# Kernel optimization log

Measured on AMD Instinct MI355X. Metric: run time of the kernel, lower is better.

## Reference

```python
import jax, jax.numpy as jnp
import numpy as np

EPS = 1e-12  # torch F.normalize default eps


def _l2norm(x):
    # F.normalize(x, dim=-1): x / max(||x||_2, eps)
    n = jnp.sqrt(jnp.sum(x * x, axis=-1, keepdims=True))
    return x / jnp.maximum(n, EPS)


def setup_inputs() -> dict:
    key = jax.random.key(0)
    ks = jax.random.split(key, 5)
    n, d, t, h = 16, 1024, 1024, 4
    dh = d // h
    return {
        "rgb": jax.random.normal(ks[0], (n, d, t), dtype=jnp.float32),
        "flow": jax.random.normal(ks[1], (n, d, t), dtype=jnp.float32),
        "rgb_proj": jax.random.normal(ks[2], (h, d, dh), dtype=jnp.float32),
        "flow_proj": jax.random.normal(ks[3], (h, d, dh), dtype=jnp.float32),
        "atte_w": jax.random.normal(ks[4], (h, dh, dh), dtype=jnp.float32),
    }


def reference(rgb, flow, rgb_proj, flow_proj, atte_w):
    # inputs are (n, d, t); module transposes to (n, t, d)
    rgb_t = jnp.swapaxes(rgb, -1, -2)
    flow_t = jnp.swapaxes(flow, -1, -2)
    n, t, d = rgb_t.shape

    # per-head projection + L2 normalize: (n, h, t, dh)
    o_rgb = _l2norm(jnp.einsum('ntd,hde->nhte', rgb_t, rgb_proj))
    o_flow = _l2norm(jnp.einsum('ntd,hde->nhte', flow_t, flow_proj))

    # bilinear attention core: (n, h, t, t)
    att = jnp.einsum('nhte,nhse->nhts', jnp.einsum('nhtd,hde->nhte', o_rgb, atte_w), o_flow)

    rgb_atte = jax.nn.softmax(att, axis=-1)
    flow_atte = jax.nn.softmax(jnp.swapaxes(att, -1, -2), axis=-1)

    e_rgb = jax.nn.gelu(jnp.einsum('nhts,nhsd->nhtd', rgb_atte, o_rgb), approximate=False)
    e_flow = jax.nn.gelu(jnp.einsum('nhts,nhsd->nhtd', flow_atte, o_flow), approximate=False)

    # replicate torch: e.mT.reshape(n, t, -1) (C-order reinterpretation of (n,h,dh,t))
    f_rgb = jnp.tanh(jnp.swapaxes(e_rgb, -1, -2).reshape(n, t, d) + rgb_t)
    f_flow = jnp.tanh(jnp.swapaxes(e_flow, -1, -2).reshape(n, t, d) + flow_t)

    return jnp.swapaxes(f_rgb, -1, -2), jnp.swapaxes(f_flow, -1, -2)
```

## Files before the change

### kernel.cpp

```cpp
#include <hip/hip_runtime.h>
#include <hip/hip_bf16.h>
#include <cstdint>
#include <cstddef>


typedef __bf16 bf16_t;
typedef bf16_t bf16x4 __attribute__((ext_vector_type(4)));
typedef bf16_t bf16x8 __attribute__((ext_vector_type(8)));
typedef float  f32x4  __attribute__((ext_vector_type(4)));

#define DEV static __device__ __forceinline__

constexpr int Tdim = 1024;
constexpr int Ddim = 1024;
constexpr int DH   = 256;
constexpr int NH   = 4;
constexpr int NB   = 16;

DEV f32x4 mm16(bf16x8 a, bf16x8 b, f32x4 c) {
  return __builtin_amdgcn_mfma_f32_16x16x32_bf16(a, b, c, 0, 0, 0);
}

DEV bf16x8 cmb(bf16x4 lo, bf16x4 hi) {
  return __builtin_shufflevector(lo, hi, 0, 1, 2, 3, 4, 5, 6, 7);
}

DEV void tr_pair(const bf16_t* base, int lane, bf16x4& lo, bf16x4& hi) {
  uint32_t a = (uint32_t)(uintptr_t)base + (uint32_t)(lane * 8);
  asm volatile("ds_read_b64_tr_b16 %0, %2\n\t"
               "ds_read_b64_tr_b16 %1, %2 offset:512"
               : "=v"(lo), "=v"(hi)
               : "v"(a));
}

DEV void lgkm0_fence() {
  asm volatile("s_waitcnt lgkmcnt(0)" ::: "memory");
  __builtin_amdgcn_sched_barrier(0);
}

DEV void gload16(const void* g, void* l) {
  __builtin_amdgcn_global_load_lds(
      (const __attribute__((address_space(1))) uint32_t*)g,
      (__attribute__((address_space(3))) uint32_t*)l, 16, 0, 0);
}

DEV float ftanh(float x) {
  float a = __expf(2.0f * x);
  return 1.0f - 2.0f * __builtin_amdgcn_rcpf(a + 1.0f);
}

__global__ void kconvW(const float* __restrict__ rgbp,
                       const float* __restrict__ flowp,
                       const float* __restrict__ attw,
                       bf16_t* __restrict__ Wl, bf16_t* __restrict__ Wa) {
  int bid = blockIdx.x;
  if (bid < 1024) {
    int oc = bid * 256 + threadIdx.x;
    int c = oc & 15, g = (oc >> 4) & 3, nf = (oc >> 6) & 15;
    int kb = (oc >> 10) & 31, h = (oc >> 15) & 3, mod = oc >> 17;
    const float* src = (mod ? flowp : rgbp) + (size_t)h * Ddim * DH + nf * 16 + c;
    bf16x8 v;
#pragma unroll
    for (int i = 0; i < 8; ++i) {
      int k = kb * 32 + ((i < 4) ? 4 * g + i : 12 + 4 * g + i);
      v[i] = (bf16_t)src[(size_t)k * DH];
    }
    *(bf16x8*)(Wl + (size_t)oc * 8) = v;
  } else {
    int oc = (bid - 1024) * 256 + threadIdx.x;
    int c = oc & 15, g = (oc >> 4) & 3, nf = (oc >> 6) & 15;
    int kb = (oc >> 10) & 7, h = oc >> 13;
    const float* src = attw + (size_t)h * DH * DH + nf * 16 + c;
    bf16x8 v;
#pragma unroll
    for (int i = 0; i < 8; ++i) {
      int k = kb * 32 + 8 * g + i;
      v[i] = (bf16_t)src[(size_t)k * DH];
    }
    *(bf16x8*)(Wa + (size_t)oc * 8) = v;
  }
}

__global__ __launch_bounds__(256, 4)
void kproj(const float* __restrict__ rgb, const float* __restrict__ flow,
           const bf16_t* __restrict__ Wl, const bf16_t* __restrict__ Wa,
           bf16_t* __restrict__ o_rgb, bf16_t* __restrict__ o_flow,
           bf16_t* __restrict__ Aout) {
  const int t0  = blockIdx.x * 64;
  const int h   = blockIdx.y;
  const int nn  = blockIdx.z >> 1;
  const int mod = blockIdx.z & 1;
  const float* X = (mod ? flow : rgb) + (size_t)nn * Ddim * Tdim + t0;
  const bf16_t* Wb = Wl + (size_t)(mod * NH + h) * 32 * 8192;
  bf16_t* O = (mod ? o_flow : o_rgb) + (size_t)(nn * NH + h) * Tdim * DH;

  __shared__ __align__(128) bf16_t Alds[64 * 256];
  __shared__ __align__(128) bf16_t AchD[2 * 2048];
  char* WdB = (char*)Alds;
  float* sqp = (float*)AchD;

  const int tid = threadIdx.x;
  const int lane = tid & 63, wv = tid >> 6;
  const int g = lane >> 4, ln = lane & 15;

  f32x4 acc[4][4] = {};
  const int akk = tid >> 3, atoff = (tid & 7) * 8;

  auto stageW = [&](int b, int kb) {
    const char* ws = (const char*)(Wb + (size_t)kb * 8192);
#pragma unroll
    for (int j = 0; j < 4; ++j)
      gload16(ws + j * 4096 + wv * 1024 + lane * 16,
              WdB + b * 16384 + j * 4096 + wv * 1024);
  };

  auto stageX = [&](int b, int kb) {
    const float* srcx = X + (size_t)(kb * 32 + akk) * Tdim + atoff;
    float4 f0 = *(const float4*)srcx;
    float4 f1 = *(const float4*)(srcx + 4);
    bf16x8 v = {(bf16_t)f0.x, (bf16_t)f0.y, (bf16_t)f0.z, (bf16_t)f0.w,
                (bf16_t)f1.x, (bf16_t)f1.y, (bf16_t)f1.z, (bf16_t)f1.w};
    *(bf16x8*)&AchD[b * 2048 + (atoff >> 4) * 512 + akk * 16 + (atoff & 15)] = v;
  };

  stageW(0, 0);
  __builtin_amdgcn_sched_barrier(0);
  stageX(0, 0);
  __syncthreads();

  int cur = 0;
  for (int kb = 0; kb < 32; ++kb) {
    if (kb + 1 < 32) {
      stageW(cur ^ 1, kb + 1);
      __builtin_amdgcn_sched_barrier(0);
      stageX(cur ^ 1, kb + 1);
    }

    bf16x4 alo[4], ahi[4];
#pragma unroll
    for (int mi = 0; mi < 4; ++mi)
      tr_pair(&AchD[cur * 2048 + mi * 512], lane, alo[mi], ahi[mi]);
    bf16x8 wf[4];
#pragma unroll
    for (int f = 0; f < 4; ++f)
      wf[f] = *(const bf16x8*)(WdB + cur * 16384 + (wv * 4 + f) * 1024 +
                               lane * 16);
    lgkm0_fence();
#pragma unroll
    for (int mi = 0; mi < 4; ++mi) {
      bf16x8 a = cmb(alo[mi], ahi[mi]);
#pragma unroll
      for (int f = 0; f < 4; ++f) acc[mi][f] = mm16(a, wf[f], acc[mi][f]);
    }
    __syncthreads();
    cur ^= 1;
  }

  float inv[4][4];
#pragma unroll
  for (int mi = 0; mi < 4; ++mi)
#pragma unroll
    for (int r = 0; r < 4; ++r) {
      float s = 0.f;
#pragma unroll
      for (int f = 0; f < 4; ++f) { float v = acc[mi][f][r]; s += v * v; }
      s += __shfl_xor(s, 1); s += __shfl_xor(s, 2);
      s += __shfl_xor(s, 4); s += __shfl_xor(s, 8);
      if (ln == 0) sqp[wv * 64 + mi * 16 + 4 * g + r] = s;
    }
  __syncthreads();
#pragma unroll
  for (int mi = 0; mi < 4; ++mi)
#pragma unroll
    for (int r = 0; r < 4; ++r) {
      int rl = mi * 16 + 4 * g + r;
      float s = sqp[rl] + sqp[64 + rl] + sqp[128 + rl] + sqp[192 + rl];
      inv[mi][r] = 1.0f / fmaxf(sqrtf(s), 1e-12f);
    }
  __syncthreads();

#pragma unroll
  for (int mi = 0; mi < 4; ++mi)
#pragma unroll
    for (int f = 0; f < 4; ++f)
#pragma unroll
      for (int r = 0; r < 4; ++r) {
        bf16_t val = (bf16_t)(acc[mi][f][r] * inv[mi][r]);
        int row = mi * 16 + 4 * g + r;
        int col = wv * 64 + f * 16 + ln;
        O[(size_t)(t0 + row) * DH + col] = val;
        if (mod == 0)
          *(bf16_t*)((char*)Alds + ((row * 512 + col * 2) ^ ((row & 7) << 4))) = val;
      }

  if (mod != 0) return;

  __syncthreads();
  bf16_t* Ao = Aout + (size_t)(nn * NH + h) * Tdim * DH;
  f32x4 acc2[4][4] = {};
  for (int kb = 0; kb < 8; ++kb) {
    bf16x8 af[4];
#pragma unroll
    for (int mi = 0; mi < 4; ++mi) {
      int row = mi * 16 + ln;
      af[mi] = *(const bf16x8*)((const char*)Alds +
               ((row * 512 + kb * 64 + g * 16) ^ ((row & 7) << 4)));
    }
    bf16x8 wf[4];
    const bf16_t* wt = Wa + (size_t)(h * 8 + kb) * 8192 + (wv * 4) * 512 + lane * 8;
#pragma unroll
    for (int f = 0; f < 4; ++f) wf[f] = *(const bf16x8*)(wt + f * 512);
#pragma unroll
    for (int mi = 0; mi < 4; ++mi)
#pragma unroll
      for (int f = 0; f < 4; ++f) acc2[mi][f] = mm16(af[mi], wf[f], acc2[mi][f]);
  }
#pragma unroll
  for (int mi = 0; mi < 4; ++mi)
#pragma unroll
    for (int f = 0; f < 4; ++f)
#pragma unroll
      for (int r = 0; r < 4; ++r)
        Ao[(size_t)(t0 + mi * 16 + 4 * g + r) * DH + wv * 64 + f * 16 + ln] =
            (bf16_t)acc2[mi][f][r];
}

__global__ __launch_bounds__(256, 2)
void kflash(const bf16_t* __restrict__ o_rgb, const bf16_t* __restrict__ o_flow,
            const bf16_t* __restrict__ Aw,
            const float* __restrict__ rgb, const float* __restrict__ flow,
            float* __restrict__ out) {
  const int bid = blockIdx.x;
  const int p  = (bid & 7) * 16 + (bid >> 6);
  const int qx = (bid >> 3) & 7;
  const int nn = p >> 3, h = (p >> 1) & 3, pass = p & 1;
  const int t0 = qx * 128;
  const size_t nhoff = (size_t)(nn * NH + h) * Tdim * DH;
  const bf16_t* Qp = (pass ? o_flow : Aw) + nhoff;
  const bf16_t* Kp = (pass ? Aw : o_flow) + nhoff;
  const bf16_t* Vp = (pass ? o_flow : o_rgb) + nhoff;
  const float*  Xr = (pass ? flow : rgb) + (size_t)nn * Ddim * Tdim;
  float* Op = out + (size_t)pass * NB * Ddim * Tdim + (size_t)nn * Ddim * Tdim;

  __shared__ __align__(128) bf16_t Klds[2][32 * 256];
  __shared__ __align__(128) bf16_t Vch [2][32 * 256];

  const int tid = threadIdx.x;
  const int lane = tid & 63, wv = tid >> 6;
  const int g = lane >> 4, ln = lane & 15;

  bf16x8 qf[2][8];
#pragma unroll
  for (int rg = 0; rg < 2; ++rg) {
    const bf16_t* qrow = Qp + (size_t)(t0 + wv * 32 + rg * 16 + ln) * DH;
#pragma unroll
    for (int ks = 0; ks < 8; ++ks)
      qf[rg][ks] = *(const bf16x8*)(qrow + ks * 32 + 8 * g);
  }

  auto stage = [&](int b, int s0) {
    const char* Ks = (const char*)Kp + (size_t)s0 * 512;
    const char* Vs = (const char*)Vp + (size_t)s0 * 512;
    char* Kd = (char*)&Klds[b][0] + wv * 1024;
    char* Vd = (char*)&Vch[b][0] + wv * 1024;
#pragma unroll
    for (int j = 0; j < 4; ++j) {
      int gc = j * 256 + tid;
      int d  = gc * 16;
      gload16(Ks + (d ^ (((d >> 9) & 7) << 4)), Kd + j * 4096);
      int ech = gc >> 6, kk = (gc & 63) >> 1, half = gc & 1;
      gload16(Vs + kk * 512 + (ech * 2 + half) * 16, Vd + j * 4096);
    }
  };

  f32x4 eacc[2][16] = {};
  float l_par[2] = {0.f, 0.f};

  stage(0, 0);
  __syncthreads();

  int cur = 0;
  for (int s0 = 0; s0 < Tdim; s0 += 32) {
    if (s0 + 32 < Tdim) stage(cur ^ 1, s0 + 32);

    f32x4 sacc[2][2] = {};
#pragma unroll
    for (int ks = 0; ks < 8; ++ks) {
      int row0 = ln, row1 = 16 + ln;
      bf16x8 kf0 = *(const bf16x8*)((const char*)&Klds[cur][0] +
          ((row0 * 512 + ks * 64 + g * 16) ^ ((row0 & 7) << 4)));
      bf16x8 kf1 = *(const bf16x8*)((const char*)&Klds[cur][0] +
          ((row1 * 512 + ks * 64 + g * 16) ^ ((row1 & 7) << 4)));
      sacc[0][0] = mm16(kf0, qf[0][ks], sacc[0][0]);
      sacc[1][0] = mm16(kf0, qf[1][ks], sacc[1][0]);
      sacc[0][1] = mm16(kf1, qf[0][ks], sacc[0][1]);
      sacc[1][1] = mm16(kf1, qf[1][ks], sacc[1][1]);
    }

    bf16x8 pa[2];
#pragma unroll
    for (int rg = 0; rg < 2; ++rg) {
      bf16x4 lo, hi;
#pragma unroll
      for (int r = 0; r < 4; ++r) {
        float p0 = __expf(sacc[rg][0][r] - 8.0f);
        float p1 = __expf(sacc[rg][1][r] - 8.0f);
        l_par[rg] += p0 + p1;
        lo[r] = (bf16_t)p0;
        hi[r] = (bf16_t)p1;
      }
      pa[rg] = cmb(lo, hi);
    }

#pragma unroll
    for (int nb4 = 0; nb4 < 4; ++nb4) {
      bf16x4 vlo[4], vhi[4];
#pragma unroll
      for (int j = 0; j < 4; ++j)
        tr_pair(&Vch[cur][(nb4 * 4 + j) * 512], lane, vlo[j], vhi[j]);
      lgkm0_fence();
#pragma unroll
      for (int j = 0; j < 4; ++j) {
        bf16x8 vf = cmb(vlo[j], vhi[j]);
        eacc[0][nb4 * 4 + j] = mm16(pa[0], vf, eacc[0][nb4 * 4 + j]);
        eacc[1][nb4 * 4 + j] = mm16(pa[1], vf, eacc[1][nb4 * 4 + j]);
      }
    }

    __syncthreads();
    cur ^= 1;
  }

  float invl[2][4];
#pragma unroll
  for (int rg = 0; rg < 2; ++rg) {
    float l = l_par[rg];
    l += __shfl_xor(l, 16); l += __shfl_xor(l, 32);
#pragma unroll
    for (int r = 0; r < 4; ++r)
      invl[rg][r] = 1.0f / __shfl(l, 4 * g + r, 16);
  }
#pragma unroll
  for (int rg = 0; rg < 2; ++rg)
#pragma unroll
    for (int nb = 0; nb < 16; ++nb)
#pragma unroll
      for (int r = 0; r < 4; ++r) {
        float e = eacc[rg][nb][r] * invl[rg][r];
        float u = 0.79788456f * (e + 0.044715f * e * e * e);
        float ge = 0.5f * e * (1.0f + ftanh(u));
        int trow = t0 + wv * 32 + rg * 16 + 4 * g + r;
        int col = h * 256 + nb * 16 + ln;
        size_t idx = (size_t)trow * Tdim + col;
        Op[idx] = ftanh(ge + Xr[idx]);
      }
}

extern "C" void kernel_launch(void* const* d_in, const int* in_sizes, int n_in,
                              void* d_out, int out_size, void* d_ws, size_t ws_size,
                              hipStream_t stream) {
  const float* rgb   = (const float*)d_in[0];
  const float* flow  = (const float*)d_in[1];
  const float* rgbp  = (const float*)d_in[2];
  const float* flowp = (const float*)d_in[3];
  const float* attw  = (const float*)d_in[4];
  float* out = (float*)d_out;

  const size_t OSZ = (size_t)NB * NH * Tdim * DH;
  bf16_t* o_rgb  = (bf16_t*)d_ws;
  bf16_t* o_flow = o_rgb + OSZ;
  bf16_t* Aw     = o_flow + OSZ;
  bf16_t* Wl     = Aw + OSZ;
  bf16_t* Wa     = Wl + (size_t)2 * NH * 32 * 8192;

  kconvW<<<1152, 256, 0, stream>>>(rgbp, flowp, attw, Wl, Wa);
  kproj<<<dim3(16, 4, 32), 256, 0, stream>>>(rgb, flow, Wl, Wa,
                                             o_rgb, o_flow, Aw);
  kflash<<<1024, 256, 0, stream>>>(o_rgb, o_flow, Aw, rgb, flow, out);
}
```

Before: 331.0 us.

## Double kproj token tile to 128 and register-prefetch X loads

The projection kernel now processes 128 tokens per block instead of 64. This halves the number of blocks and doubles reuse of each staged weight tile. X loads for the next k-block are issued into registers before the MFMAs and written to LDS after them, overlapping global latency with compute. The LDS layout is merged into one buffer, and occupancy drops to 2 blocks per CU, which raises register pressure from the larger accumulators.

```diff
diff --git a/kernel.cpp b/kernel.cpp
--- a/kernel.cpp
+++ b/kernel.cpp
@@ -81,12 +81,12 @@
   }
 }
 
-__global__ __launch_bounds__(256, 4)
+__global__ __launch_bounds__(256, 2)
 void kproj(const float* __restrict__ rgb, const float* __restrict__ flow,
            const bf16_t* __restrict__ Wl, const bf16_t* __restrict__ Wa,
            bf16_t* __restrict__ o_rgb, bf16_t* __restrict__ o_flow,
            bf16_t* __restrict__ Aout) {
-  const int t0  = blockIdx.x * 64;
+  const int t0  = blockIdx.x * 128;
   const int h   = blockIdx.y;
   const int nn  = blockIdx.z >> 1;
   const int mod = blockIdx.z & 1;
@@ -94,17 +94,18 @@
   const bf16_t* Wb = Wl + (size_t)(mod * NH + h) * 32 * 8192;
   bf16_t* O = (mod ? o_flow : o_rgb) + (size_t)(nn * NH + h) * Tdim * DH;
 
-  __shared__ __align__(128) bf16_t Alds[64 * 256];
-  __shared__ __align__(128) bf16_t AchD[2 * 2048];
+  __shared__ __align__(128) bf16_t Alds[128 * 256];
   char* WdB = (char*)Alds;
-  float* sqp = (float*)AchD;
+  bf16_t* AchD = Alds + 16384;
+  float* sqp = (float*)(Alds + 16384);
 
   const int tid = threadIdx.x;
   const int lane = tid & 63, wv = tid >> 6;
   const int g = lane >> 4, ln = lane & 15;
 
-  f32x4 acc[4][4] = {};
-  const int akk = tid >> 3, atoff = (tid & 7) * 8;
+  f32x4 acc[8][4] = {};
+  const int akk = tid >> 3;
+  const int atc = tid & 7;
 
   auto stageW = [&](int b, int kb) {
     const char* ws = (const char*)(Wb + (size_t)kb * 8192);
@@ -114,32 +115,45 @@
               WdB + b * 16384 + j * 4096 + wv * 1024);
   };
 
-  auto stageX = [&](int b, int kb) {
-    const float* srcx = X + (size_t)(kb * 32 + akk) * Tdim + atoff;
-    float4 f0 = *(const float4*)srcx;
-    float4 f1 = *(const float4*)(srcx + 4);
-    bf16x8 v = {(bf16_t)f0.x, (bf16_t)f0.y, (bf16_t)f0.z, (bf16_t)f0.w,
-                (bf16_t)f1.x, (bf16_t)f1.y, (bf16_t)f1.z, (bf16_t)f1.w};
-    *(bf16x8*)&AchD[b * 2048 + (atoff >> 4) * 512 + akk * 16 + (atoff & 15)] = v;
+  auto loadX = [&](int kb, float4* xr) {
+    const float* srcx = X + (size_t)(kb * 32 + akk) * Tdim + atc * 16;
+#pragma unroll
+    for (int j = 0; j < 4; ++j) xr[j] = *(const float4*)(srcx + j * 4);
   };
-
-  stageW(0, 0);
-  __builtin_amdgcn_sched_barrier(0);
-  stageX(0, 0);
+  auto writeX = [&](int b, const float4* xr) {
+#pragma unroll
+    for (int half = 0; half < 2; ++half) {
+      bf16x8 v = {(bf16_t)xr[2 * half].x,     (bf16_t)xr[2 * half].y,
+                  (bf16_t)xr[2 * half].z,     (bf16_t)xr[2 * half].w,
+                  (bf16_t)xr[2 * half + 1].x, (bf16_t)xr[2 * half + 1].y,
+                  (bf16_t)xr[2 * half + 1].z, (bf16_t)xr[2 * half + 1].w};
+      *(bf16x8*)&AchD[b * 4096 + atc * 512 + akk * 16 + half * 8] = v;
+    }
+  };
+
+  {
+    float4 x0[4];
+    loadX(0, x0);
+    __builtin_amdgcn_sched_barrier(0);
+    stageW(0, 0);
+    __builtin_amdgcn_sched_barrier(0);
+    writeX(0, x0);
+  }
   __syncthreads();
 
   int cur = 0;
   for (int kb = 0; kb < 32; ++kb) {
-    if (kb + 1 < 32) {
-      stageW(cur ^ 1, kb + 1);
-      __builtin_amdgcn_sched_barrier(0);
-      stageX(cur ^ 1, kb + 1);
-    }
-
-    bf16x4 alo[4], ahi[4];
-#pragma unroll
-    for (int mi = 0; mi < 4; ++mi)
-      tr_pair(&AchD[cur * 2048 + mi * 512], lane, alo[mi], ahi[mi]);
+    float4 xn[4];
+    const bool nxt = (kb + 1 < 32);
+    if (nxt) loadX(kb + 1, xn);
+    __builtin_amdgcn_sched_barrier(0);
+    if (nxt) stageW(cur ^ 1, kb + 1);
+    __builtin_amdgcn_sched_barrier(0);
+
+    bf16x4 alo[8], ahi[8];
+#pragma unroll
+    for (int mi = 0; mi < 8; ++mi)
+      tr_pair(&AchD[cur * 4096 + mi * 512], lane, alo[mi], ahi[mi]);
     bf16x8 wf[4];
 #pragma unroll
     for (int f = 0; f < 4; ++f)
@@ -147,18 +161,20 @@
                                lane * 16);
     lgkm0_fence();
 #pragma unroll
-    for (int mi = 0; mi < 4; ++mi) {
+    for (int mi = 0; mi < 8; ++mi) {
       bf16x8 a = cmb(alo[mi], ahi[mi]);
 #pragma unroll
       for (int f = 0; f < 4; ++f) acc[mi][f] = mm16(a, wf[f], acc[mi][f]);
     }
+
+    if (nxt) writeX(cur ^ 1, xn);
     __syncthreads();
     cur ^= 1;
   }
 
-  float inv[4][4];
-#pragma unroll
-  for (int mi = 0; mi < 4; ++mi)
+  float inv[8][4];
+#pragma unroll
+  for (int mi = 0; mi < 8; ++mi)
 #pragma unroll
     for (int r = 0; r < 4; ++r) {
       float s = 0.f;
@@ -166,21 +182,21 @@
       for (int f = 0; f < 4; ++f) { float v = acc[mi][f][r]; s += v * v; }
       s += __shfl_xor(s, 1); s += __shfl_xor(s, 2);
       s += __shfl_xor(s, 4); s += __shfl_xor(s, 8);
-      if (ln == 0) sqp[wv * 64 + mi * 16 + 4 * g + r] = s;
-    }
-  __syncthreads();
-#pragma unroll
-  for (int mi = 0; mi < 4; ++mi)
+      if (ln == 0) sqp[wv * 128 + mi * 16 + 4 * g + r] = s;
+    }
+  __syncthreads();
+#pragma unroll
+  for (int mi = 0; mi < 8; ++mi)
 #pragma unroll
     for (int r = 0; r < 4; ++r) {
       int rl = mi * 16 + 4 * g + r;
-      float s = sqp[rl] + sqp[64 + rl] + sqp[128 + rl] + sqp[192 + rl];
+      float s = sqp[rl] + sqp[128 + rl] + sqp[256 + rl] + sqp[384 + rl];
       inv[mi][r] = 1.0f / fmaxf(sqrtf(s), 1e-12f);
     }
   __syncthreads();
 
 #pragma unroll
-  for (int mi = 0; mi < 4; ++mi)
+  for (int mi = 0; mi < 8; ++mi)
 #pragma unroll
     for (int f = 0; f < 4; ++f)
 #pragma unroll
@@ -197,11 +213,11 @@
 
   __syncthreads();
   bf16_t* Ao = Aout + (size_t)(nn * NH + h) * Tdim * DH;
-  f32x4 acc2[4][4] = {};
+  f32x4 acc2[8][4] = {};
   for (int kb = 0; kb < 8; ++kb) {
-    bf16x8 af[4];
-#pragma unroll
-    for (int mi = 0; mi < 4; ++mi) {
+    bf16x8 af[8];
+#pragma unroll
+    for (int mi = 0; mi < 8; ++mi) {
       int row = mi * 16 + ln;
       af[mi] = *(const bf16x8*)((const char*)Alds +
                ((row * 512 + kb * 64 + g * 16) ^ ((row & 7) << 4)));
@@ -211,12 +227,12 @@
 #pragma unroll
     for (int f = 0; f < 4; ++f) wf[f] = *(const bf16x8*)(wt + f * 512);
 #pragma unroll
-    for (int mi = 0; mi < 4; ++mi)
+    for (int mi = 0; mi < 8; ++mi)
 #pragma unroll
       for (int f = 0; f < 4; ++f) acc2[mi][f] = mm16(af[mi], wf[f], acc2[mi][f]);
   }
 #pragma unroll
-  for (int mi = 0; mi < 4; ++mi)
+  for (int mi = 0; mi < 8; ++mi)
 #pragma unroll
     for (int f = 0; f < 4; ++f)
 #pragma unroll
@@ -374,7 +390,7 @@
   bf16_t* Wa     = Wl + (size_t)2 * NH * 32 * 8192;
 
   kconvW<<<1152, 256, 0, stream>>>(rgbp, flowp, attw, Wl, Wa);
-  kproj<<<dim3(16, 4, 32), 256, 0, stream>>>(rgb, flow, Wl, Wa,
-                                             o_rgb, o_flow, Aw);
+  kproj<<<dim3(8, 4, 32), 256, 0, stream>>>(rgb, flow, Wl, Wa,
+                                            o_rgb, o_flow, Aw);
   kflash<<<1024, 256, 0, stream>>>(o_rgb, o_flow, Aw, rgb, flow, out);
 }
```

After: 329.5 us. No clear change (-0.5%).
